# Kernel tuning notes

Hardware: AMD Instinct MI355X
Metric: run time of the kernel (lower is better)

Reference implementation:

```python
import jax, jax.numpy as jnp
import numpy as np
from jax import lax

# --- model constants (match init_kwargs) ---
B = 4096
T, N_FEAT = 100, 81
KH = 7                 # cnn_kernel_height
T_MOD = T - KH + 1     # 94
M = 100                # cnn_hidden_size
P = 128                # decoder hidden size
SKIP = 10
SH = 32                # skip_hidden_size
PT = T_MOD // SKIP     # 9


def setup_inputs() -> dict:
    key = jax.random.key(0)
    ks = jax.random.split(key, 18)
    s = 0.05
    def rn(k, shape, scale=s):
        return jax.random.normal(k, shape, dtype=jnp.float32) * scale
    return {
        "enc_data": jax.random.normal(ks[0], (B, T, N_FEAT), dtype=jnp.float32),
        # Conv2d(1 -> M, kernel=(KH, N_FEAT))
        "conv_w": rn(ks[1], (M, 1, KH, N_FEAT)),
        "conv_b": rn(ks[2], (M,)),
        # TemporalAttention: W_d: Linear(2P->M, no bias), U_d: Linear(M->M, no bias), v_d: Linear(M->1, no bias)
        "Wd": rn(ks[3], (M, 2 * P)),
        "Ud": rn(ks[4], (M, M)),
        "vd": rn(ks[5], (1, M)),
        # LSTM(input=M, hidden=P), PyTorch gate order i,f,g,o
        "lstm_wih": rn(ks[6], (4 * P, M)),
        "lstm_whh": rn(ks[7], (4 * P, P)),
        "lstm_bih": rn(ks[8], (4 * P,)),
        "lstm_bhh": rn(ks[9], (4 * P,)),
        # GRU(input=M, hidden=SH), PyTorch gate order r,z,n
        "gru_wih": rn(ks[10], (3 * SH, M)),
        "gru_whh": rn(ks[11], (3 * SH, SH)),
        "gru_bih": rn(ks[12], (3 * SH,)),
        "gru_bhh": rn(ks[13], (3 * SH,)),
        # output head: Linear(M+P+SKIP*SH -> P), ReLU, (Dropout=eval identity), Linear(P -> 1)
        "out1_w": rn(ks[14], (P, M + P + SKIP * SH)),
        "out1_b": rn(ks[15], (P,)),
        "out2_w": rn(ks[16], (1, P)),
        "out2_b": rn(ks[17], (1,)),
    }


def reference(enc_data, conv_w, conv_b, Wd, Ud, vd,
              lstm_wih, lstm_whh, lstm_bih, lstm_bhh,
              gru_wih, gru_whh, gru_bih, gru_bhh,
              out1_w, out1_b, out2_w, out2_b):
    b = enc_data.shape[0]

    # --- CNN encoder: Conv2d valid over full feature width -> [B, T_MOD, M] ---
    x = enc_data[:, None]  # [B,1,T,n]
    h = lax.conv_general_dilated(x, conv_w, window_strides=(1, 1), padding='VALID',
                                 dimension_numbers=('NCHW', 'OIHW', 'NCHW'))  # [B,M,T_MOD,1]
    H = jax.nn.relu(h + conv_b[None, :, None, None])[..., 0].transpose(0, 2, 1)  # [B,T_MOD,M]

    # precompute U_d(H) once (same math; U_d applied to H is step-invariant)
    HU = jnp.einsum('btm,km->btk', H, Ud)  # [B,T_MOD,M]

    def dec_step(carry, _):
        d, s = carry  # each [B,P]
        q = jnp.concatenate([d, s], axis=1)                       # [B,2P]
        e = jnp.tanh((q @ Wd.T)[:, None, :] + HU)                 # [B,T_MOD,M]
        scores = jnp.einsum('btm,m->bt', e, vd[0])                # [B,T_MOD]
        beta = jax.nn.softmax(scores, axis=1)                     # softmax over time
        c = jnp.einsum('bt,btm->bm', beta, H)                     # context [B,M]
        gates = c @ lstm_wih.T + lstm_bih + d @ lstm_whh.T + lstm_bhh
        i_g, f_g, g_g, o_g = jnp.split(gates, 4, axis=1)
        s_new = jax.nn.sigmoid(f_g) * s + jax.nn.sigmoid(i_g) * jnp.tanh(g_g)
        d_new = jax.nn.sigmoid(o_g) * jnp.tanh(s_new)
        return (d_new, s_new), (beta, c)

    d0 = jnp.zeros((b, P), dtype=enc_data.dtype)
    s0 = jnp.zeros((b, P), dtype=enc_data.dtype)
    (d_T, _), (betas, cs) = lax.scan(dec_step, (d0, s0), None, length=T_MOD)
    c_last = cs[-1]                                               # [B,M]
    dec_out = jnp.concatenate([d_T, c_last], axis=1)              # [B, P+M]

    # --- skip GRU over strided conv features ---
    Hs = H[:, -PT * SKIP:, :]                                     # [B, PT*SKIP, M]
    Hs = (Hs.transpose(0, 2, 1)                                   # [B, M, PT*SKIP]
            .reshape(b, M, PT, SKIP)
            .transpose(2, 0, 3, 1)                                # [PT, B, SKIP, M]
            .reshape(PT, b * SKIP, M))

    def gru_step(hprev, xt):
        gi = xt @ gru_wih.T + gru_bih
        gh = hprev @ gru_whh.T + gru_bhh
        ir, iz, inn = jnp.split(gi, 3, axis=1)
        hr, hz, hn = jnp.split(gh, 3, axis=1)
        r = jax.nn.sigmoid(ir + hr)
        z = jax.nn.sigmoid(iz + hz)
        nn_ = jnp.tanh(inn + r * hn)
        hnew = (1.0 - z) * nn_ + z * hprev
        return hnew, None

    h0 = jnp.zeros((b * SKIP, SH), dtype=enc_data.dtype)
    h_skip, _ = lax.scan(gru_step, h0, Hs)                        # [B*SKIP, SH]
    h_skip = h_skip.reshape(b, SKIP * SH)                         # matches torch view

    feat = jnp.concatenate([dec_out, h_skip], axis=1)             # [B, P+M+SKIP*SH]
    out = jax.nn.relu(feat @ out1_w.T + out1_b) @ out2_w.T + out2_b  # [B,1]
    return out[:, 0]
```

## Files before the change

kernel.cpp:

```cpp
#include <hip/hip_runtime.h>

typedef unsigned int u32;
typedef unsigned short u16;
typedef _Float16 half2_t __attribute__((ext_vector_type(2)));

#define TM 94
#define NB 4
#define DEC_NT 1024

__device__ __forceinline__ float bf2f(u16 v){ return __builtin_bit_cast(float, ((u32)v)<<16); }
__device__ __forceinline__ float bflo(u32 v){ return __builtin_bit_cast(float, v<<16); }
__device__ __forceinline__ float bfhi(u32 v){ return __builtin_bit_cast(float, v & 0xffff0000u); }
__device__ __forceinline__ u32 f2bf_bits(float f){ u32 u=__builtin_bit_cast(u32,f); return (u + 0x7fffu + ((u>>16)&1u))>>16; }
__device__ __forceinline__ u32 packbf2(float a, float b){ return f2bf_bits(a) | (f2bf_bits(b)<<16); }
__device__ __forceinline__ u32 packh2(float a, float b){ half2_t h; h.x=(_Float16)a; h.y=(_Float16)b; return __builtin_bit_cast(u32,h); }
__device__ __forceinline__ float fdot2(u32 a, u32 b, float c){
  return __builtin_amdgcn_fdot2(__builtin_bit_cast(half2_t,a), __builtin_bit_cast(half2_t,b), c, false);
}
__device__ __forceinline__ float fast_rcp(float x){ return __builtin_amdgcn_rcpf(x); }
__device__ __forceinline__ float sigmoid_f(float x){ return fast_rcp(1.f + __expf(-x)); }
__device__ __forceinline__ float tanh_f(float x){ float e=__expf(2.f*x); return 1.f - 2.f*fast_rcp(e+1.f); }

__global__ __launch_bounds__(128)
void conv_kernel(const float* __restrict__ enc, const float* __restrict__ cw,
                 const float* __restrict__ cb, u16* __restrict__ Hb)
{
  __shared__ float sE[8100];
  const int tid = threadIdx.x;
  const int b = blockIdx.y;
  const int chunk = blockIdx.x;
  const float* ep = enc + (size_t)b*8100;
  for (int i=tid;i<8100;i+=128) sE[i]=ep[i];
  __syncthreads();
  if (tid >= TM) return;
  const int t = tid;
  const int mo = chunk*10;
  const float* wb = cw + mo*567;
  float acc[10];
  #pragma unroll
  for (int k=0;k<10;k++) acc[k]=cb[mo+k];
  const float* e = sE + t*81;
  #pragma unroll 3
  for (int j=0;j<567;j++){
    float ev = e[j];
    #pragma unroll
    for (int k=0;k<10;k++) acc[k] += ev*wb[k*567+j];
  }
  u32* out = (u32*)Hb + ((size_t)b*9400 + t*100 + mo)/2;
  #pragma unroll
  for (int k=0;k<5;k++) out[k] = packbf2(fmaxf(acc[2*k],0.f), fmaxf(acc[2*k+1],0.f));
}

#define OFF_SHU 75200
#define OFF_SQ2 150400
#define OFF_SC2 152448
#define OFF_SVD 153280
#define OFF_AB  153680
#define DEC_LDS 161872

__global__ __launch_bounds__(DEC_NT, 4)
__attribute__((amdgpu_waves_per_eu(4, 4)))
void decoder_kernel(const u16* __restrict__ Hb, const float* __restrict__ Wd,
                    const float* __restrict__ Ud, const float* __restrict__ vd,
                    const float* __restrict__ wih, const float* __restrict__ whh,
                    const float* __restrict__ bih, const float* __restrict__ bhh,
                    float* __restrict__ dT, float* __restrict__ cLast)
{
  extern __shared__ char smem[];
  u16*      sH   = (u16*)smem;
  u16*      sHU  = (u16*)(smem + OFF_SHU);
  _Float16* sq2  = (_Float16*)(smem + OFF_SQ2);
  u32*      sc2  = (u32*)(smem + OFF_SC2);
  float*    svd  = (float*)(smem + OFF_SVD);
  float*    sa   = (float*)(smem + OFF_AB);
  float*    sbeta= (float*)(smem + OFF_AB + 1600);
  _Float16* sgA  = (_Float16*)(smem + OFF_AB);
  _Float16* sgB  = (_Float16*)(smem + OFF_AB + 4096);

  const int tid = threadIdx.x;
  const int b0 = blockIdx.x * NB;

  {
    const uint4* src = (const uint4*)(Hb + (size_t)b0*9400);
    uint4* dst = (uint4*)sH;
    for (int i=tid;i<4700;i+=DEC_NT) dst[i]=src[i];
  }
  if (tid < 100) svd[tid] = vd[tid];
  {
    u32* q2 = (u32*)sq2;
    for (int i=tid;i<NB*128;i+=DEC_NT) q2[i]=0u;
  }
  __syncthreads();

  for (int idx=tid; idx<9400; idx+=DEC_NT){
    int kq = idx/376;
    int r  = idx - kq*376;
    int bi = r/94;
    int t  = r - 94*bi;
    const u32* hrow = (const u32*)sH + bi*4700 + t*50;
    const float* ud0 = Ud + (kq*4+0)*100;
    const float* ud1 = Ud + (kq*4+1)*100;
    const float* ud2 = Ud + (kq*4+2)*100;
    const float* ud3 = Ud + (kq*4+3)*100;
    float c0=0.f,c1=0.f,c2=0.f,c3=0.f;
    #pragma unroll 5
    for (int mq=0; mq<25; mq++){
      uint2 hp = *(const uint2*)(hrow + mq*2);
      float h0=bflo(hp.x), h1=bfhi(hp.x), h2=bflo(hp.y), h3=bfhi(hp.y);
      float4 u0 = *(const float4*)(ud0 + mq*4);
      float4 u1 = *(const float4*)(ud1 + mq*4);
      float4 u2 = *(const float4*)(ud2 + mq*4);
      float4 u3 = *(const float4*)(ud3 + mq*4);
      c0 += h0*u0.x + h1*u0.y + h2*u0.z + h3*u0.w;
      c1 += h0*u1.x + h1*u1.y + h2*u1.z + h3*u1.w;
      c2 += h0*u2.x + h1*u2.y + h2*u2.z + h3*u2.w;
      c3 += h0*u3.x + h1*u3.y + h2*u3.z + h3*u3.w;
    }
    u32* dst = (u32*)sHU + bi*4700 + t*50 + kq*2;
    dst[0] = packbf2(c0,c1);
    dst[1] = packbf2(c2,c3);
  }
  __syncthreads();
  __builtin_amdgcn_sched_barrier(0);

  const int half = tid >> 9;
  const int g    = tid & 511;
  u32 WA[58];
  float biasg = 0.f;
  if (half == 0){
    const float2* wr = (const float2*)(wih + (size_t)g*100);
    #pragma unroll
    for (int i=0;i<50;i++){ float2 v = wr[i]; WA[i]=packh2(v.x,v.y); }
    const float2* hr = (const float2*)(whh + (size_t)g*128);
    #pragma unroll
    for (int i=0;i<8;i++){ float2 v = hr[i]; WA[50+i]=packh2(v.x,v.y); }
    biasg = bih[g] + bhh[g];
  } else {
    const float2* hr = (const float2*)(whh + (size_t)g*128 + 16);
    #pragma unroll
    for (int i=0;i<56;i++){ float2 v = hr[i]; WA[i]=packh2(v.x,v.y); }
  }
  const int mw = tid>>3, part = tid&7;
  u32 Wdf[16];
  if (mw < 100){
    const float* wd = Wd + mw*256 + part*32;
    #pragma unroll
    for (int i=0;i<4;i++){
      int ii = (i+part)&3;
      #pragma unroll
      for (int k=0;k<4;k++){
        Wdf[4*i+k] = packh2(wd[ii*8+2*k], wd[ii*8+2*k+1]);
      }
    }
  }

  float s_reg = 0.f;

  for (int step=0; step<TM; step++){
    if (mw < 100){
      #pragma unroll 1
      for (int bi=0;bi<NB;bi++){
        const u32* qb = (const u32*)sq2 + bi*128 + part*16;
        float a0=0.f, a1=0.f;
        #pragma unroll
        for (int i=0;i<4;i++){
          int ii = (i+part)&3;
          uint4 qv = *(const uint4*)(qb + ii*4);
          a0 = fdot2(Wdf[4*i+0], qv.x, a0);
          a1 = fdot2(Wdf[4*i+1], qv.y, a1);
          a0 = fdot2(Wdf[4*i+2], qv.z, a0);
          a1 = fdot2(Wdf[4*i+3], qv.w, a1);
        }
        float acc = a0+a1;
        acc += __shfl_xor(acc,1);
        acc += __shfl_xor(acc,2);
        acc += __shfl_xor(acc,4);
        if (part==0) sa[bi*100+mw]=acc;
      }
    }
    __syncthreads();
    if (tid < 752){
      int row = tid>>1, th = tid&1;
      int bi = row/94;
      int t  = row - 94*bi;
      const uint4* hu4 = (const uint4*)((const u32*)sHU + bi*4700 + t*50 + th*24);
      const float4* ap = (const float4*)(sa + bi*100) + th*12;
      const float4* vp = (const float4*)svd + th*12;
      float acc=0.f;
      #pragma unroll
      for (int c=0;c<6;c++){
        uint4 h4 = hu4[c];
        float4 a0 = ap[2*c], a1 = ap[2*c+1];
        float4 v0 = vp[2*c], v1 = vp[2*c+1];
        acc += v0.x*tanh_f(a0.x + bflo(h4.x));
        acc += v0.y*tanh_f(a0.y + bfhi(h4.x));
        acc += v0.z*tanh_f(a0.z + bflo(h4.y));
        acc += v0.w*tanh_f(a0.w + bfhi(h4.y));
        acc += v1.x*tanh_f(a1.x + bflo(h4.z));
        acc += v1.y*tanh_f(a1.y + bfhi(h4.z));
        acc += v1.z*tanh_f(a1.z + bflo(h4.w));
        acc += v1.w*tanh_f(a1.w + bfhi(h4.w));
      }
      if (th){
        uint2 ht = *(const uint2*)((const u32*)hu4 + 24);
        float4 a = ap[12]; float4 v = vp[12];
        acc += v.x*tanh_f(a.x + bflo(ht.x));
        acc += v.y*tanh_f(a.y + bfhi(ht.x));
        acc += v.z*tanh_f(a.z + bflo(ht.y));
        acc += v.w*tanh_f(a.w + bfhi(ht.y));
      }
      acc += __shfl_xor(acc,1);
      if (!th) sbeta[bi*96+t]=acc;
    }
    __syncthreads();
    if (tid < 64*NB){
      int bi = tid>>6, lane = tid&63;
      float s0 = sbeta[bi*96+lane];
      float s1 = (lane<30)? sbeta[bi*96+64+lane] : -1e30f;
      float mx = fmaxf(s0,s1);
      #pragma unroll
      for (int o=32;o>=1;o>>=1) mx = fmaxf(mx, __shfl_xor(mx,o));
      float e0 = __expf(s0-mx);
      float e1 = (lane<30)? __expf(s1-mx) : 0.f;
      float sm = e0+e1;
      #pragma unroll
      for (int o=32;o>=1;o>>=1) sm += __shfl_xor(sm,o);
      float rs = fast_rcp(sm);
      sbeta[bi*96+lane] = e0*rs;
      if (lane<30) sbeta[bi*96+64+lane] = e1*rs;
    }
    __syncthreads();
    if (tid < 800){
      int bi = tid/200;
      int r  = tid - 200*bi;
      int mp = r>>2, th = r&3;
      int tstart = (th<2) ? th*24 : 48+(th-2)*23;
      const float* bp = sbeta + bi*96 + tstart;
      const u32* hp = (const u32*)sH + bi*4700 + tstart*50 + mp;
      float a0=0.f, a1=0.f;
      #pragma unroll
      for (int i=0;i<23;i++){
        float be = bp[i];
        u32 h = hp[i*50];
        a0 += be*bflo(h); a1 += be*bfhi(h);
      }
      if (th<2){
        float be = bp[23]; u32 h = hp[23*50];
        a0 += be*bflo(h); a1 += be*bfhi(h);
      }
      a0 += __shfl_xor(a0,1); a1 += __shfl_xor(a1,1);
      a0 += __shfl_xor(a0,2); a1 += __shfl_xor(a1,2);
      if (th==0){
        sc2[bi*52+mp] = packh2(a0,a1);
        if (step==TM-1){
          cLast[(size_t)(b0+bi)*100 + 2*mp]   = a0;
          cLast[(size_t)(b0+bi)*100 + 2*mp+1] = a1;
        }
      }
    }
    __syncthreads();
    if (half == 0){
      #pragma unroll 1
      for (int bi=0;bi<NB;bi++){
        float a0 = biasg, a1 = 0.f;
        const uint4* cp = (const uint4*)(sc2 + bi*52);
        #pragma unroll
        for (int i=0;i<12;i++){
          uint4 cv = cp[i];
          a0 = fdot2(WA[4*i+0], cv.x, a0);
          a1 = fdot2(WA[4*i+1], cv.y, a1);
          a0 = fdot2(WA[4*i+2], cv.z, a0);
          a1 = fdot2(WA[4*i+3], cv.w, a1);
        }
        {
          const u32* ct = sc2 + bi*52 + 48;
          a0 = fdot2(WA[48], ct[0], a0);
          a1 = fdot2(WA[49], ct[1], a1);
        }
        const uint4* qp = (const uint4*)((const u32*)sq2 + bi*128);
        #pragma unroll
        for (int i=0;i<2;i++){
          uint4 qv = qp[i];
          a0 = fdot2(WA[50+4*i+0], qv.x, a0);
          a1 = fdot2(WA[50+4*i+1], qv.y, a1);
          a0 = fdot2(WA[50+4*i+2], qv.z, a0);
          a1 = fdot2(WA[50+4*i+3], qv.w, a1);
        }
        sgA[bi*512+g] = (_Float16)(a0+a1);
      }
    } else {
      #pragma unroll 1
      for (int bi=0;bi<NB;bi++){
        float a0 = 0.f, a1 = 0.f;
        const uint4* qp = (const uint4*)((const u32*)sq2 + bi*128);
        #pragma unroll
        for (int i=0;i<14;i++){
          uint4 qv = qp[2+i];
          a0 = fdot2(WA[4*i+0], qv.x, a0);
          a1 = fdot2(WA[4*i+1], qv.y, a1);
          a0 = fdot2(WA[4*i+2], qv.z, a0);
          a1 = fdot2(WA[4*i+3], qv.w, a1);
        }
        sgB[bi*512+g] = (_Float16)(a0+a1);
      }
    }
    __syncthreads();
    if (tid < 512){
      int bi = tid>>7, p = tid&127;
      float ig = (float)sgA[bi*512+p]       + (float)sgB[bi*512+p];
      float fg = (float)sgA[bi*512+128+p]   + (float)sgB[bi*512+128+p];
      float gg = (float)sgA[bi*512+256+p]   + (float)sgB[bi*512+256+p];
      float og = (float)sgA[bi*512+384+p]   + (float)sgB[bi*512+384+p];
      float sn = sigmoid_f(fg)*s_reg + sigmoid_f(ig)*tanh_f(gg);
      float dn = sigmoid_f(og)*tanh_f(sn);
      s_reg = sn;
      sq2[bi*256+p]=(_Float16)dn;
      sq2[bi*256+128+p]=(_Float16)sn;
      if (step==TM-1) dT[(size_t)(b0+bi)*128+p]=dn;
    }
    __syncthreads();
  }
}

__global__ __launch_bounds__(256)
void gru_kernel(const u16* __restrict__ Hb, const float* __restrict__ wih,
                const float* __restrict__ whh, const float* __restrict__ bihp,
                const float* __restrict__ bhhp, float* __restrict__ hskip)
{
  __shared__ float sWih[96][101];
  __shared__ float sWhh[96][33];
  __shared__ float sxt[8][100];
  __shared__ float sh[8][33];
  const int tid = threadIdx.x;
  for (int i=tid;i<9600;i+=256){ sWih[i/100][i%100]=wih[i]; }
  for (int i=tid;i<3072;i+=256){ sWhh[i>>5][i&31]=whh[i]; }
  const int r = tid>>5, j = tid&31;
  const int rowg = blockIdx.x*8 + r;
  const int b = rowg/10, sk = rowg - b*10;
  const float b_r = bihp[j], b_z = bihp[32+j], b_n = bihp[64+j];
  const float hb_r = bhhp[j], hb_z = bhhp[32+j], hb_n = bhhp[64+j];
  sh[r][j]=0.f;
  float h = 0.f;
  __syncthreads();
  for (int pt=0; pt<9; pt++){
    for (int i=tid;i<800;i+=256){
      int rr=i/100, m=i-rr*100;
      int rg = blockIdx.x*8+rr; int bb=rg/10, ss=rg-bb*10;
      sxt[rr][m] = bf2f(Hb[(size_t)bb*9400 + (size_t)(4+pt*10+ss)*100 + m]);
    }
    __syncthreads();
    float gi_r=b_r, gi_z=b_z, gi_n=b_n, gh_r=hb_r, gh_z=hb_z, gh_n=hb_n;
    #pragma unroll 4
    for (int m=0;m<100;m++){
      float x = sxt[r][m];
      gi_r += sWih[j][m]*x; gi_z += sWih[32+j][m]*x; gi_n += sWih[64+j][m]*x;
    }
    #pragma unroll
    for (int k=0;k<32;k++){
      float hp = sh[r][k];
      gh_r += sWhh[j][k]*hp; gh_z += sWhh[32+j][k]*hp; gh_n += sWhh[64+j][k]*hp;
    }
    float rg_ = sigmoid_f(gi_r+gh_r);
    float z  = sigmoid_f(gi_z+gh_z);
    float n  = tanh_f(gi_n + rg_*gh_n);
    h = (1.f-z)*n + z*h;
    __syncthreads();
    sh[r][j]=h;
    __syncthreads();
  }
  hskip[(size_t)b*320 + sk*32 + j] = h;
}

#define OUT_NB 32
#define OUT_LDS ((OUT_NB*552 + 8*552)*4)

__global__ __launch_bounds__(256)
void out_kernel(const float* __restrict__ dT, const float* __restrict__ cLast,
                const float* __restrict__ hskip, const float* __restrict__ w1,
                const float* __restrict__ b1, const float* __restrict__ w2,
                const float* __restrict__ b2, float* __restrict__ outp)
{
  extern __shared__ float osm[];
  float* sf = osm;
  float* sw = osm + OUT_NB*552;
  const int tid = threadIdx.x;
  const int b0 = blockIdx.x*OUT_NB;
  for (int i=tid;i<OUT_NB*548;i+=256){
    int bl = i/548, k = i - 548*bl; int b = b0+bl;
    float v;
    if (k<128) v = dT[(size_t)b*128+k];
    else if (k<228) v = cLast[(size_t)b*100+(k-128)];
    else v = hskip[(size_t)b*320+(k-228)];
    sf[bl*552+k]=v;
  }
  const int bl = tid>>3, j = tid&7;
  float outv = 0.f;
  for (int jt=0; jt<128; jt+=8){
    __syncthreads();
    for (int i=tid;i<8*548;i+=256){
      int rr=i/548, c=i-548*rr;
      sw[rr*552+c] = w1[(size_t)jt*548 + i];
    }
    __syncthreads();
    float acc = b1[jt+j];
    const float* fr = sf + bl*552;
    const float* wr = sw + j*552;
    #pragma unroll 4
    for (int k=0;k<548;k++) acc += fr[k]*wr[k];
    outv += fmaxf(acc,0.f)*w2[jt+j];
  }
  outv += __shfl_xor(outv,1);
  outv += __shfl_xor(outv,2);
  outv += __shfl_xor(outv,4);
  if (j==0) outp[b0+bl] = outv + b2[0];
}

extern "C" void kernel_launch(void* const* d_in, const int* in_sizes, int n_in,
                              void* d_out, int out_size, void* d_ws, size_t ws_size,
                              hipStream_t stream)
{
  const float* enc      = (const float*)d_in[0];
  const float* conv_w   = (const float*)d_in[1];
  const float* conv_b   = (const float*)d_in[2];
  const float* Wd       = (const float*)d_in[3];
  const float* Ud       = (const float*)d_in[4];
  const float* vd       = (const float*)d_in[5];
  const float* lstm_wih = (const float*)d_in[6];
  const float* lstm_whh = (const float*)d_in[7];
  const float* lstm_bih = (const float*)d_in[8];
  const float* lstm_bhh = (const float*)d_in[9];
  const float* gru_wih  = (const float*)d_in[10];
  const float* gru_whh  = (const float*)d_in[11];
  const float* gru_bih  = (const float*)d_in[12];
  const float* gru_bhh  = (const float*)d_in[13];
  const float* out1_w   = (const float*)d_in[14];
  const float* out1_b   = (const float*)d_in[15];
  const float* out2_w   = (const float*)d_in[16];
  const float* out2_b   = (const float*)d_in[17];

  char* ws = (char*)d_ws;
  u16*   Hb    = (u16*)ws;
  float* dT    = (float*)(ws + 77004800);
  float* cLast = (float*)(ws + 79101952);
  float* hskip = (float*)(ws + 80740352);

  conv_kernel<<<dim3(10,4096,1), 128, 0, stream>>>(enc, conv_w, conv_b, Hb);

  (void)hipFuncSetAttribute((const void*)decoder_kernel,
                            hipFuncAttributeMaxDynamicSharedMemorySize, DEC_LDS);
  decoder_kernel<<<4096/NB, DEC_NT, DEC_LDS, stream>>>(Hb, Wd, Ud, vd,
                                                       lstm_wih, lstm_whh, lstm_bih, lstm_bhh,
                                                       dT, cLast);

  gru_kernel<<<5120, 256, 0, stream>>>(Hb, gru_wih, gru_whh, gru_bih, gru_bhh, hskip);

  (void)hipFuncSetAttribute((const void*)out_kernel,
                            hipFuncAttributeMaxDynamicSharedMemorySize, OUT_LDS);
  out_kernel<<<4096/OUT_NB, 256, OUT_LDS, stream>>>(dT, cLast, hskip, out1_w, out1_b,
                                                    out2_w, out2_b, (float*)d_out);
}
```

Baseline: 7.632 ms.

## Stream pre-packed fp16 LSTM weights from global memory instead of holding them in registers

A new prep kernel packs the LSTM input and recurrent weights into fp16 pairs laid out as interleaved uint4 columns. The decoder no longer keeps 58 packed weight registers per thread. Each step it streams these weights from global or L2 with a two-deep prefetch and computes all four batch rows per weight load over a unified z vector [c; d] in LDS. This frees registers and drops the waves_per_eu constraint, at the cost of re-reading the weights from cache every timestep. WgT aliases the hskip workspace region, which the later GRU kernel overwrites after the decoder has finished.

```diff
diff --git a/kernel.cpp b/kernel.cpp
--- a/kernel.cpp
+++ b/kernel.cpp
@@ -20,6 +20,26 @@
 __device__ __forceinline__ float fast_rcp(float x){ return __builtin_amdgcn_rcpf(x); }
 __device__ __forceinline__ float sigmoid_f(float x){ return fast_rcp(1.f + __expf(-x)); }
 __device__ __forceinline__ float tanh_f(float x){ float e=__expf(2.f*x); return 1.f - 2.f*fast_rcp(e+1.f); }
+
+__global__ __launch_bounds__(256)
+void prep_kernel(const float* __restrict__ wih, const float* __restrict__ whh,
+                 uint4* __restrict__ WgT)
+{
+  int idx = blockIdx.x*256 + threadIdx.x;
+  int t = idx & 1023;
+  int j = idx >> 10;
+  int h = t >> 9, g = t & 511;
+  u32 r[4];
+  #pragma unroll
+  for (int s=0;s<4;s++){
+    int u = 4*j + s;
+    u32 v = 0u;
+    if (h==0){ if (u < 50) v = packh2(wih[g*100+2*u], wih[g*100+2*u+1]); }
+    else     { if (u < 64) v = packh2(whh[g*128+2*u], whh[g*128+2*u+1]); }
+    r[s]=v;
+  }
+  WgT[idx] = make_uint4(r[0],r[1],r[2],r[3]);
+}
 
 __global__ __launch_bounds__(128)
 void conv_kernel(const float* __restrict__ enc, const float* __restrict__ cw,
@@ -52,25 +72,26 @@
 }
 
 #define OFF_SHU 75200
-#define OFF_SQ2 150400
-#define OFF_SC2 152448
-#define OFF_SVD 153280
-#define OFF_AB  153680
-#define DEC_LDS 161872
-
-__global__ __launch_bounds__(DEC_NT, 4)
-__attribute__((amdgpu_waves_per_eu(4, 4)))
+#define OFF_SQ  150400
+#define OFF_SZ  152448
+#define OFF_SVD 154496
+#define OFF_AB  154896
+#define DEC_LDS 163088
+
+__global__ __launch_bounds__(DEC_NT, 2)
 void decoder_kernel(const u16* __restrict__ Hb, const float* __restrict__ Wd,
                     const float* __restrict__ Ud, const float* __restrict__ vd,
-                    const float* __restrict__ wih, const float* __restrict__ whh,
+                    const uint4* __restrict__ WgT,
                     const float* __restrict__ bih, const float* __restrict__ bhh,
                     float* __restrict__ dT, float* __restrict__ cLast)
 {
   extern __shared__ char smem[];
   u16*      sH   = (u16*)smem;
   u16*      sHU  = (u16*)(smem + OFF_SHU);
-  _Float16* sq2  = (_Float16*)(smem + OFF_SQ2);
-  u32*      sc2  = (u32*)(smem + OFF_SC2);
+  u32*      sq32 = (u32*)(smem + OFF_SQ);
+  _Float16* sq16 = (_Float16*)(smem + OFF_SQ);
+  u32*      sz32 = (u32*)(smem + OFF_SZ);
+  _Float16* sz16 = (_Float16*)(smem + OFF_SZ);
   float*    svd  = (float*)(smem + OFF_SVD);
   float*    sa   = (float*)(smem + OFF_AB);
   float*    sbeta= (float*)(smem + OFF_AB + 1600);
@@ -86,10 +107,7 @@
     for (int i=tid;i<4700;i+=DEC_NT) dst[i]=src[i];
   }
   if (tid < 100) svd[tid] = vd[tid];
-  {
-    u32* q2 = (u32*)sq2;
-    for (int i=tid;i<NB*128;i+=DEC_NT) q2[i]=0u;
-  }
+  for (int i=tid;i<NB*128;i+=DEC_NT){ sq32[i]=0u; sz32[i]=0u; }
   __syncthreads();
 
   for (int idx=tid; idx<9400; idx+=DEC_NT){
@@ -121,25 +139,7 @@
     dst[1] = packbf2(c2,c3);
   }
   __syncthreads();
-  __builtin_amdgcn_sched_barrier(0);
-
-  const int half = tid >> 9;
-  const int g    = tid & 511;
-  u32 WA[58];
-  float biasg = 0.f;
-  if (half == 0){
-    const float2* wr = (const float2*)(wih + (size_t)g*100);
-    #pragma unroll
-    for (int i=0;i<50;i++){ float2 v = wr[i]; WA[i]=packh2(v.x,v.y); }
-    const float2* hr = (const float2*)(whh + (size_t)g*128);
-    #pragma unroll
-    for (int i=0;i<8;i++){ float2 v = hr[i]; WA[50+i]=packh2(v.x,v.y); }
-    biasg = bih[g] + bhh[g];
-  } else {
-    const float2* hr = (const float2*)(whh + (size_t)g*128 + 16);
-    #pragma unroll
-    for (int i=0;i<56;i++){ float2 v = hr[i]; WA[i]=packh2(v.x,v.y); }
-  }
+
   const int mw = tid>>3, part = tid&7;
   u32 Wdf[16];
   if (mw < 100){
@@ -153,14 +153,19 @@
       }
     }
   }
+  const int gh = tid >> 9, gg = tid & 511;
+  const float biasg = (gh==0) ? (bih[gg] + bhh[gg]) : 0.f;
+  const uint4* wgp = WgT + tid;
+  const int jmax = gh ? 16 : 13;
 
   float s_reg = 0.f;
 
+  #pragma unroll 1
   for (int step=0; step<TM; step++){
     if (mw < 100){
       #pragma unroll 1
       for (int bi=0;bi<NB;bi++){
-        const u32* qb = (const u32*)sq2 + bi*128 + part*16;
+        const u32* qb = sq32 + bi*128 + part*16;
         float a0=0.f, a1=0.f;
         #pragma unroll
         for (int i=0;i<4;i++){
@@ -251,7 +256,7 @@
       a0 += __shfl_xor(a0,1); a1 += __shfl_xor(a1,1);
       a0 += __shfl_xor(a0,2); a1 += __shfl_xor(a1,2);
       if (th==0){
-        sc2[bi*52+mp] = packh2(a0,a1);
+        sz32[bi*128+mp] = packh2(a0,a1);
         if (step==TM-1){
           cLast[(size_t)(b0+bi)*100 + 2*mp]   = a0;
           cLast[(size_t)(b0+bi)*100 + 2*mp+1] = a1;
@@ -259,63 +264,48 @@
       }
     }
     __syncthreads();
-    if (half == 0){
+    {
+      float acc0 = biasg, acc1 = biasg, acc2 = biasg, acc3 = biasg;
+      uint4 w0 = wgp[0], w1 = wgp[1024];
+      const u32* zb = sz32 + gh*64;
       #pragma unroll 1
-      for (int bi=0;bi<NB;bi++){
-        float a0 = biasg, a1 = 0.f;
-        const uint4* cp = (const uint4*)(sc2 + bi*52);
-        #pragma unroll
-        for (int i=0;i<12;i++){
-          uint4 cv = cp[i];
-          a0 = fdot2(WA[4*i+0], cv.x, a0);
-          a1 = fdot2(WA[4*i+1], cv.y, a1);
-          a0 = fdot2(WA[4*i+2], cv.z, a0);
-          a1 = fdot2(WA[4*i+3], cv.w, a1);
-        }
-        {
-          const u32* ct = sc2 + bi*52 + 48;
-          a0 = fdot2(WA[48], ct[0], a0);
-          a1 = fdot2(WA[49], ct[1], a1);
-        }
-        const uint4* qp = (const uint4*)((const u32*)sq2 + bi*128);
-        #pragma unroll
-        for (int i=0;i<2;i++){
-          uint4 qv = qp[i];
-          a0 = fdot2(WA[50+4*i+0], qv.x, a0);
-          a1 = fdot2(WA[50+4*i+1], qv.y, a1);
-          a0 = fdot2(WA[50+4*i+2], qv.z, a0);
-          a1 = fdot2(WA[50+4*i+3], qv.w, a1);
-        }
-        sgA[bi*512+g] = (_Float16)(a0+a1);
-      }
-    } else {
-      #pragma unroll 1
-      for (int bi=0;bi<NB;bi++){
-        float a0 = 0.f, a1 = 0.f;
-        const uint4* qp = (const uint4*)((const u32*)sq2 + bi*128);
-        #pragma unroll
-        for (int i=0;i<14;i++){
-          uint4 qv = qp[2+i];
-          a0 = fdot2(WA[4*i+0], qv.x, a0);
-          a1 = fdot2(WA[4*i+1], qv.y, a1);
-          a0 = fdot2(WA[4*i+2], qv.z, a0);
-          a1 = fdot2(WA[4*i+3], qv.w, a1);
-        }
-        sgB[bi*512+g] = (_Float16)(a0+a1);
-      }
+      for (int j=0;j<jmax;j++){
+        uint4 wc = w0; w0 = w1;
+        int jn = (j+2<16)? j+2 : 15;
+        w1 = wgp[jn*1024];
+        const u32* z0 = zb + 4*j;
+        uint4 zv0 = *(const uint4*)(z0);
+        uint4 zv1 = *(const uint4*)(z0+128);
+        uint4 zv2 = *(const uint4*)(z0+256);
+        uint4 zv3 = *(const uint4*)(z0+384);
+        acc0 = fdot2(wc.x, zv0.x, acc0); acc0 = fdot2(wc.y, zv0.y, acc0);
+        acc0 = fdot2(wc.z, zv0.z, acc0); acc0 = fdot2(wc.w, zv0.w, acc0);
+        acc1 = fdot2(wc.x, zv1.x, acc1); acc1 = fdot2(wc.y, zv1.y, acc1);
+        acc1 = fdot2(wc.z, zv1.z, acc1); acc1 = fdot2(wc.w, zv1.w, acc1);
+        acc2 = fdot2(wc.x, zv2.x, acc2); acc2 = fdot2(wc.y, zv2.y, acc2);
+        acc2 = fdot2(wc.z, zv2.z, acc2); acc2 = fdot2(wc.w, zv2.w, acc2);
+        acc3 = fdot2(wc.x, zv3.x, acc3); acc3 = fdot2(wc.y, zv3.y, acc3);
+        acc3 = fdot2(wc.z, zv3.z, acc3); acc3 = fdot2(wc.w, zv3.w, acc3);
+      }
+      _Float16* sgp = gh ? sgB : sgA;
+      sgp[       gg] = (_Float16)acc0;
+      sgp[ 512 + gg] = (_Float16)acc1;
+      sgp[1024 + gg] = (_Float16)acc2;
+      sgp[1536 + gg] = (_Float16)acc3;
     }
     __syncthreads();
     if (tid < 512){
       int bi = tid>>7, p = tid&127;
       float ig = (float)sgA[bi*512+p]       + (float)sgB[bi*512+p];
       float fg = (float)sgA[bi*512+128+p]   + (float)sgB[bi*512+128+p];
-      float gg = (float)sgA[bi*512+256+p]   + (float)sgB[bi*512+256+p];
+      float gg_= (float)sgA[bi*512+256+p]   + (float)sgB[bi*512+256+p];
       float og = (float)sgA[bi*512+384+p]   + (float)sgB[bi*512+384+p];
-      float sn = sigmoid_f(fg)*s_reg + sigmoid_f(ig)*tanh_f(gg);
+      float sn = sigmoid_f(fg)*s_reg + sigmoid_f(ig)*tanh_f(gg_);
       float dn = sigmoid_f(og)*tanh_f(sn);
       s_reg = sn;
-      sq2[bi*256+p]=(_Float16)dn;
-      sq2[bi*256+128+p]=(_Float16)sn;
+      sq16[bi*256+p]      = (_Float16)dn;
+      sq16[bi*256+128+p]  = (_Float16)sn;
+      sz16[bi*256+128+p]  = (_Float16)dn;
       if (step==TM-1) dT[(size_t)(b0+bi)*128+p]=dn;
     }
     __syncthreads();
@@ -443,13 +433,16 @@
   float* dT    = (float*)(ws + 77004800);
   float* cLast = (float*)(ws + 79101952);
   float* hskip = (float*)(ws + 80740352);
+  uint4* WgT   = (uint4*)(ws + 80740352);
+
+  prep_kernel<<<64, 256, 0, stream>>>(lstm_wih, lstm_whh, WgT);
 
   conv_kernel<<<dim3(10,4096,1), 128, 0, stream>>>(enc, conv_w, conv_b, Hb);
 
   (void)hipFuncSetAttribute((const void*)decoder_kernel,
                             hipFuncAttributeMaxDynamicSharedMemorySize, DEC_LDS);
-  decoder_kernel<<<4096/NB, DEC_NT, DEC_LDS, stream>>>(Hb, Wd, Ud, vd,
-                                                       lstm_wih, lstm_whh, lstm_bih, lstm_bhh,
+  decoder_kernel<<<4096/NB, DEC_NT, DEC_LDS, stream>>>(Hb, Wd, Ud, vd, WgT,
+                                                       lstm_bih, lstm_bhh,
                                                        dT, cLast);
 
   gru_kernel<<<5120, 256, 0, stream>>>(Hb, gru_wih, gru_whh, gru_bih, gru_bhh, hskip);
```

After: 7.544 ms. About the same (-1.2%).
